# Performance work log

Measured on AMD Instinct MI355X. Metric: run time of the kernel, lower is better.

Reference implementation:

```python
import jax, jax.numpy as jnp
import numpy as np

NUM_USERS = 200000
NUM_ITEMS = 100000
EMB = 64
NUM_LAYERS = 3


def setup_inputs() -> dict:
    rng = np.random.default_rng(0)
    E_INTER = 2_000_000
    # unique (user, item) interactions -> faithful to adj[e0, e1] = 1.0 set-semantics
    lin = np.unique(rng.integers(0, NUM_USERS * NUM_ITEMS, size=E_INTER, dtype=np.int64))
    u = (lin // NUM_ITEMS).astype(np.int32)
    it = (lin % NUM_ITEMS).astype(np.int32) + NUM_USERS  # item node ids offset by NUM_USERS
    row = np.concatenate([u, it])  # symmetric bipartite graph, no self-loops
    col = np.concatenate([it, u])
    edge_index = jnp.asarray(np.stack([row, col]), dtype=jnp.int32)  # [2, E]

    key = jax.random.key(0)
    k1, k2 = jax.random.split(key)
    # xavier_uniform on nn.Embedding.weight
    bu = float(np.sqrt(6.0 / (NUM_USERS + EMB)))
    bi = float(np.sqrt(6.0 / (NUM_ITEMS + EMB)))
    user_emb = jax.random.uniform(k1, (NUM_USERS, EMB), jnp.float32, -bu, bu)
    item_emb = jax.random.uniform(k2, (NUM_ITEMS, EMB), jnp.float32, -bi, bi)
    return {"edge_index": edge_index, "user_emb": user_emb, "item_emb": item_emb}


def reference(edge_index, user_emb, item_emb):
    num_users = user_emb.shape[0]
    N = num_users + item_emb.shape[0]
    x = jnp.concatenate([user_emb, item_emb], axis=0)  # ego embeddings [N, D]
    row, col = edge_index[0], edge_index[1]

    # adj has unique off-diagonal edges + eye(N): row-sum degree = edge count + 1
    deg = jax.ops.segment_sum(jnp.ones(row.shape, x.dtype), row, num_segments=N) + 1.0
    dinv = jax.lax.rsqrt(deg)                 # deg >= 1, never inf
    w = (dinv[row] * dinv[col])[:, None]      # per-edge D^-1/2 A D^-1/2 weight
    self_w = (dinv * dinv)[:, None]           # self-loop weight d_i^-1

    acc = x  # sum over layer outputs, including layer 0
    for _ in range(NUM_LAYERS):
        x = jax.ops.segment_sum(w * x[col], row, num_segments=N) + self_w * x
        # dropout is identity in eval mode
        acc = acc + x

    return acc[:num_users], acc[num_users:]
```

## Files before the change

kernel.cpp:

```cpp
#include <hip/hip_runtime.h>
#include <hip/hip_bf16.h>

#define EMB 64
#define BKT_BITS 10
#define BKT_SZ   (1 << BKT_BITS)
#define U_BITS   18
#define U_MASK   ((1u << U_BITS) - 1u)

__device__ __forceinline__ float bf2f(unsigned short h) {
    return __uint_as_float(((unsigned)h) << 16);
}
__device__ __forceinline__ unsigned short f2bf(float f) {
    unsigned u = __float_as_uint(f);
    unsigned r = (u + 0x7fffu + ((u >> 16) & 1u)) >> 16;
    return (unsigned short)r;
}

__global__ void k1_kernel(const int* __restrict__ row, const int* __restrict__ colh,
                          int* __restrict__ urp, int* __restrict__ degit,
                          int NU, int Eh, int urp_blocks) {
    if ((int)blockIdx.x < urp_blocks) {
        int r = blockIdx.x * blockDim.x + threadIdx.x;
        if (r > NU) return;
        if (r == NU) { urp[NU] = Eh; return; }
        int lo = 0, hi = Eh;
        while (lo < hi) {
            int mid = (lo + hi) >> 1;
            if (row[mid] < r) lo = mid + 1; else hi = mid;
        }
        urp[r] = lo;
    } else {
        int e = (blockIdx.x - urp_blocks) * blockDim.x + threadIdx.x;
        if (e < Eh) atomicAdd(&degit[colh[e] - NU], 1);
    }
}

__global__ void k3_kernel(const int* __restrict__ degit, int* __restrict__ excl,
                          int* __restrict__ partials,
                          const int* __restrict__ urp, float* __restrict__ dinv,
                          const float* __restrict__ ue, const float* __restrict__ ie,
                          unsigned short* __restrict__ y0,
                          int NU, int NI, int N, long nu_elems, long total,
                          int nb_s1, int nb_dv) {
    int b = blockIdx.x;
    if (b < nb_s1) {
        __shared__ int sh[256];
        int t = threadIdx.x;
        int base = b * 1024 + t * 4;
        int d0 = (base + 0 < NI) ? degit[base + 0] : 0;
        int d1 = (base + 1 < NI) ? degit[base + 1] : 0;
        int d2 = (base + 2 < NI) ? degit[base + 2] : 0;
        int d3 = (base + 3 < NI) ? degit[base + 3] : 0;
        int tsum = d0 + d1 + d2 + d3;
        sh[t] = tsum;
        __syncthreads();
        for (int off = 1; off < 256; off <<= 1) {
            int v = (t >= off) ? sh[t - off] : 0;
            __syncthreads();
            sh[t] += v;
            __syncthreads();
        }
        int excl_t = sh[t] - tsum;
        if (base + 0 < NI) excl[base + 0] = excl_t;
        if (base + 1 < NI) excl[base + 1] = excl_t + d0;
        if (base + 2 < NI) excl[base + 2] = excl_t + d0 + d1;
        if (base + 3 < NI) excl[base + 3] = excl_t + d0 + d1 + d2;
        if (t == 255) partials[b] = sh[t];
    } else if (b < nb_s1 + nb_dv) {
        int i = (b - nb_s1) * blockDim.x + threadIdx.x;
        if (i >= N) return;
        int d = (i < NU) ? (urp[i + 1] - urp[i]) : degit[i - NU];
        dinv[i] = rsqrtf((float)d + 1.0f);
    } else {
        long j4 = ((long)(b - nb_s1 - nb_dv) * blockDim.x + threadIdx.x) * 4;
        if (j4 >= total) return;
        int node = (int)(j4 >> 6);
        int d = (node < NU) ? (urp[node + 1] - urp[node]) : degit[node - NU];
        float sc = rsqrtf((float)d + 1.0f);
        float4 v = (j4 < nu_elems) ? ((const float4*)ue)[j4 >> 2]
                                   : ((const float4*)ie)[(j4 - nu_elems) >> 2];
        ushort4 o;
        o.x = f2bf(sc * v.x); o.y = f2bf(sc * v.y);
        o.z = f2bf(sc * v.z); o.w = f2bf(sc * v.w);
        ((ushort4*)y0)[j4 >> 2] = o;
    }
}

__global__ void scan2_kernel(int* __restrict__ partials, int nb) {
    __shared__ int sh[512];
    int t = threadIdx.x;
    int v = (t < nb) ? partials[t] : 0;
    sh[t] = v;
    __syncthreads();
    for (int off = 1; off < 512; off <<= 1) {
        int u = (t >= off) ? sh[t - off] : 0;
        __syncthreads();
        sh[t] += u;
        __syncthreads();
    }
    if (t < nb) partials[t] = sh[t] - v;
}

__global__ void scan3_kernel(const int* __restrict__ excl, const int* __restrict__ partials,
                             int* __restrict__ irp, int* __restrict__ cursor,
                             int* __restrict__ bcur, int NI, int Eh) {
    int i = blockIdx.x * blockDim.x + threadIdx.x;
    if (i < NI) {
        int v = excl[i] + partials[i >> 10];
        irp[i] = v;
        cursor[i] = v;
        if ((i & (BKT_SZ - 1)) == 0) bcur[i >> BKT_BITS] = v;
    }
    if (i == NI) irp[NI] = Eh;
}

__global__ void passA_kernel(const int* __restrict__ rowh, const int* __restrict__ colh,
                             int* __restrict__ bcur, unsigned* __restrict__ staging,
                             int Eh, int NU, int NB) {
    __shared__ int cnt[512];
    __shared__ int base[512];
    int t = threadIdx.x;
    for (int j = t; j < NB; j += 256) cnt[j] = 0;
    __syncthreads();
    long cb = (long)blockIdx.x * 1024;
    int b[4], rk[4];
    unsigned pk[4];
#pragma unroll
    for (int j = 0; j < 4; ++j) {
        long e = cb + j * 256 + t;
        if (e < Eh) {
            int u = rowh[e];
            int loc = colh[e] - NU;
            b[j] = loc >> BKT_BITS;
            pk[j] = ((unsigned)(loc & (BKT_SZ - 1)) << U_BITS) | (unsigned)u;
            rk[j] = atomicAdd(&cnt[b[j]], 1);
        } else {
            b[j] = -1;
        }
    }
    __syncthreads();
    for (int j = t; j < NB; j += 256)
        base[j] = cnt[j] ? atomicAdd(&bcur[j], cnt[j]) : 0;
    __syncthreads();
#pragma unroll
    for (int j = 0; j < 4; ++j)
        if (b[j] >= 0) staging[base[b[j]] + rk[j]] = pk[j];
}

__device__ __forceinline__ void spmm_node_l0u(
    int i, int q,
    const int* __restrict__ urp, const int* __restrict__ colg,
    const float* __restrict__ dinv,
    const unsigned short* __restrict__ yc,
    unsigned short* __restrict__ yn) {
    int s = urp[i], e = urp[i + 1];
    float di = dinv[i];
    const ushort4* __restrict__ yc4 = (const ushort4*)yc;
    long p = (long)i * 16 + q;
    ushort4 sv = yc4[p];

    float ax = 0.f, ay = 0.f, az = 0.f, aw = 0.f;
    for (int k0 = s; k0 < e; k0 += 8) {
        int   c[8];
        float w[8];
#pragma unroll
        for (int j = 0; j < 8; ++j) {
            int k = k0 + j;
            bool v = (k < e);
            c[j] = v ? colg[k] : 0;
            w[j] = v ? 1.0f : 0.0f;
        }
        ushort4 u[8];
#pragma unroll
        for (int j = 0; j < 8; ++j) u[j] = yc4[(long)c[j] * 16 + q];
#pragma unroll
        for (int j = 0; j < 8; ++j) {
            ax += w[j] * bf2f(u[j].x);
            ay += w[j] * bf2f(u[j].y);
            az += w[j] * bf2f(u[j].z);
            aw += w[j] * bf2f(u[j].w);
        }
    }
    ax += bf2f(sv.x); ay += bf2f(sv.y); az += bf2f(sv.z); aw += bf2f(sv.w);
    float t = di * di;
    ushort4 o;
    o.x = f2bf(t * ax); o.y = f2bf(t * ay); o.z = f2bf(t * az); o.w = f2bf(t * aw);
    ((ushort4*)yn)[p] = o;
}

__global__ void m6_kernel(const unsigned* __restrict__ staging,
                          const int* __restrict__ irp, int* __restrict__ cursor,
                          int* __restrict__ icols, int NB, int NI,
                          const int* __restrict__ urp,
                          const int* __restrict__ colg,
                          const float* __restrict__ dinv,
                          const unsigned short* __restrict__ y0,
                          unsigned short* __restrict__ y1, int NU) {
    int b = (int)blockIdx.x;
    if (b < NB) {
        int lo = b << BKT_BITS;
        int hi = lo + BKT_SZ; if (hi > NI) hi = NI;
        int start = irp[lo], end = irp[hi];
        for (int k = start + (int)threadIdx.x; k < end; k += 256) {
            unsigned v = staging[k];
            int u   = (int)(v & U_MASK);
            int loc = lo + (int)(v >> U_BITS);
            int pos = atomicAdd(&cursor[loc], 1);
            icols[pos] = u;
        }
    } else {
        long t = (long)(b - NB) * blockDim.x + threadIdx.x;
        int i = (int)(t >> 4);
        if (i >= NU) return;
        spmm_node_l0u(i, (int)(t & 15), urp, colg, dinv, y0, y1);
    }
}

__global__ void d2_kernel(const int* __restrict__ irp, const int* __restrict__ icols,
                          const float* __restrict__ dinv,
                          const unsigned short* __restrict__ y0,
                          unsigned short* __restrict__ y1,
                          unsigned short* __restrict__ y2, int NU, int NI) {
    long t = (long)blockIdx.x * blockDim.x + threadIdx.x;
    int j = (int)(t >> 4);
    if (j >= NI) return;
    int q = (int)(t & 15);
    int i = NU + j;
    int s = irp[j], e = irp[j + 1];
    float di = dinv[i];
    const ushort4* __restrict__ y04 = (const ushort4*)y0;
    const ushort4* __restrict__ y14 = (const ushort4*)y1;
    long p = (long)i * 16 + q;
    ushort4 sv0 = y04[p];

    float a0x = 0.f, a0y = 0.f, a0z = 0.f, a0w = 0.f;
    float a1x = 0.f, a1y = 0.f, a1z = 0.f, a1w = 0.f;
    for (int k0 = s; k0 < e; k0 += 8) {
        long  off[8];
        float w[8];
#pragma unroll
        for (int jj = 0; jj < 8; ++jj) {
            int k = k0 + jj;
            bool v = (k < e);
            int c = v ? icols[k] : 0;
            off[jj] = (long)c * 16 + q;
            w[jj] = v ? 1.0f : 0.0f;
        }
        ushort4 u0[8], u1[8];
#pragma unroll
        for (int jj = 0; jj < 8; ++jj) { u0[jj] = y04[off[jj]]; u1[jj] = y14[off[jj]]; }
#pragma unroll
        for (int jj = 0; jj < 8; ++jj) {
            a0x += w[jj] * bf2f(u0[jj].x); a0y += w[jj] * bf2f(u0[jj].y);
            a0z += w[jj] * bf2f(u0[jj].z); a0w += w[jj] * bf2f(u0[jj].w);
            a1x += w[jj] * bf2f(u1[jj].x); a1y += w[jj] * bf2f(u1[jj].y);
            a1z += w[jj] * bf2f(u1[jj].z); a1w += w[jj] * bf2f(u1[jj].w);
        }
    }
    float sq = di * di;
    a0x += bf2f(sv0.x); a0y += bf2f(sv0.y); a0z += bf2f(sv0.z); a0w += bf2f(sv0.w);
    ushort4 o1;
    o1.x = f2bf(sq * a0x); o1.y = f2bf(sq * a0y);
    o1.z = f2bf(sq * a0z); o1.w = f2bf(sq * a0w);
    ((ushort4*)y1)[p] = o1;
    a1x += bf2f(o1.x); a1y += bf2f(o1.y); a1z += bf2f(o1.z); a1w += bf2f(o1.w);
    ushort4 o2;
    o2.x = f2bf(sq * a1x); o2.y = f2bf(sq * a1y);
    o2.z = f2bf(sq * a1z); o2.w = f2bf(sq * a1w);
    ((ushort4*)y2)[p] = o2;
}

__global__ void d3_kernel(const int* __restrict__ urp, const int* __restrict__ colg,
                          const float* __restrict__ dinv,
                          const unsigned short* __restrict__ y0,
                          const unsigned short* __restrict__ y1,
                          unsigned short* __restrict__ y2,
                          float* __restrict__ out, int NU) {
    long t = (long)blockIdx.x * blockDim.x + threadIdx.x;
    int i = (int)(t >> 4);
    if (i >= NU) return;
    int q = (int)(t & 15);
    int s = urp[i], e = urp[i + 1];
    float di = dinv[i];
    const ushort4* __restrict__ y04 = (const ushort4*)y0;
    const ushort4* __restrict__ y14 = (const ushort4*)y1;
    const ushort4* __restrict__ y24 = (const ushort4*)y2;
    long p = (long)i * 16 + q;
    ushort4 sv0 = y04[p];
    ushort4 sv1 = y14[p];

    float a1x = 0.f, a1y = 0.f, a1z = 0.f, a1w = 0.f;
    float a2x = 0.f, a2y = 0.f, a2z = 0.f, a2w = 0.f;
    for (int k0 = s; k0 < e; k0 += 8) {
        long  off[8];
        float w[8];
#pragma unroll
        for (int jj = 0; jj < 8; ++jj) {
            int k = k0 + jj;
            bool v = (k < e);
            int c = v ? colg[k] : 0;
            off[jj] = (long)c * 16 + q;
            w[jj] = v ? 1.0f : 0.0f;
        }
        ushort4 u1[8], u2[8];
#pragma unroll
        for (int jj = 0; jj < 8; ++jj) { u1[jj] = y14[off[jj]]; u2[jj] = y24[off[jj]]; }
#pragma unroll
        for (int jj = 0; jj < 8; ++jj) {
            a1x += w[jj] * bf2f(u1[jj].x); a1y += w[jj] * bf2f(u1[jj].y);
            a1z += w[jj] * bf2f(u1[jj].z); a1w += w[jj] * bf2f(u1[jj].w);
            a2x += w[jj] * bf2f(u2[jj].x); a2y += w[jj] * bf2f(u2[jj].y);
            a2z += w[jj] * bf2f(u2[jj].z); a2w += w[jj] * bf2f(u2[jj].w);
        }
    }
    float sq = di * di;
    a1x += bf2f(sv1.x); a1y += bf2f(sv1.y); a1z += bf2f(sv1.z); a1w += bf2f(sv1.w);
    ushort4 o2;
    o2.x = f2bf(sq * a1x); o2.y = f2bf(sq * a1y);
    o2.z = f2bf(sq * a1z); o2.w = f2bf(sq * a1w);
    ((ushort4*)y2)[p] = o2;
    a2x += bf2f(o2.x); a2y += bf2f(o2.y); a2z += bf2f(o2.z); a2w += bf2f(o2.w);
    float inv = 1.0f / di;
    float4 o;
    o.x = (bf2f(sv0.x) + bf2f(sv1.x) + bf2f(o2.x)) * inv + di * a2x;
    o.y = (bf2f(sv0.y) + bf2f(sv1.y) + bf2f(o2.y)) * inv + di * a2y;
    o.z = (bf2f(sv0.z) + bf2f(sv1.z) + bf2f(o2.z)) * inv + di * a2z;
    o.w = (bf2f(sv0.w) + bf2f(sv1.w) + bf2f(o2.w)) * inv + di * a2w;
    ((float4*)out)[p] = o;
}

__global__ void d4_kernel(const int* __restrict__ irp, const int* __restrict__ icols,
                          const float* __restrict__ dinv,
                          const unsigned short* __restrict__ y0,
                          const unsigned short* __restrict__ y1,
                          const unsigned short* __restrict__ y2,
                          float* __restrict__ out, int NU, int NI) {
    long t = (long)blockIdx.x * blockDim.x + threadIdx.x;
    int j = (int)(t >> 4);
    if (j >= NI) return;
    int q = (int)(t & 15);
    int i = NU + j;
    int s = irp[j], e = irp[j + 1];
    float di = dinv[i];
    const ushort4* __restrict__ y04 = (const ushort4*)y0;
    const ushort4* __restrict__ y14 = (const ushort4*)y1;
    const ushort4* __restrict__ y24 = (const ushort4*)y2;
    long p = (long)i * 16 + q;
    ushort4 sv0 = y04[p];
    ushort4 sv1 = y14[p];
    ushort4 sv2 = y24[p];

    float ax = 0.f, ay = 0.f, az = 0.f, aw = 0.f;
    for (int k0 = s; k0 < e; k0 += 8) {
        int   c[8];
        float w[8];
#pragma unroll
        for (int jj = 0; jj < 8; ++jj) {
            int k = k0 + jj;
            bool v = (k < e);
            c[jj] = v ? icols[k] : 0;
            w[jj] = v ? 1.0f : 0.0f;
        }
        ushort4 u[8];
#pragma unroll
        for (int jj = 0; jj < 8; ++jj) u[jj] = y24[(long)c[jj] * 16 + q];
#pragma unroll
        for (int jj = 0; jj < 8; ++jj) {
            ax += w[jj] * bf2f(u[jj].x);
            ay += w[jj] * bf2f(u[jj].y);
            az += w[jj] * bf2f(u[jj].z);
            aw += w[jj] * bf2f(u[jj].w);
        }
    }
    ax += bf2f(sv2.x); ay += bf2f(sv2.y); az += bf2f(sv2.z); aw += bf2f(sv2.w);
    float inv = 1.0f / di;
    float4 o;
    o.x = (bf2f(sv0.x) + bf2f(sv1.x) + bf2f(sv2.x)) * inv + di * ax;
    o.y = (bf2f(sv0.y) + bf2f(sv1.y) + bf2f(sv2.y)) * inv + di * ay;
    o.z = (bf2f(sv0.z) + bf2f(sv1.z) + bf2f(sv2.z)) * inv + di * az;
    o.w = (bf2f(sv0.w) + bf2f(sv1.w) + bf2f(sv2.w)) * inv + di * aw;
    ((float4*)out)[p] = o;
}

extern "C" void kernel_launch(void* const* d_in, const int* in_sizes, int n_in,
                              void* d_out, int out_size, void* d_ws, size_t ws_size,
                              hipStream_t stream) {
    const int*   edge_index = (const int*)d_in[0];
    const float* user_emb   = (const float*)d_in[1];
    const float* item_emb   = (const float*)d_in[2];
    float* out = (float*)d_out;

    const int  E  = in_sizes[0] / 2;
    const int  Eh = E / 2;
    const int  NU = in_sizes[1] / EMB;
    const int  NI = in_sizes[2] / EMB;
    const int  N  = NU + NI;
    const long total = (long)N * EMB;

    const int* row = edge_index;
    const int* col = edge_index + E;
    const int* rowh = row;
    const int* colh = col;

    int*   urp      = (int*)d_ws;
    int*   degit    = urp + (NU + 1);
    int*   excl     = degit + NI;
    int*   partials = excl + NI;
    int*   bcur     = partials + 512;
    int*   irp      = bcur + 512;
    int*   cursor   = irp + (NI + 1);
    int*   icols    = cursor + NI;
    float* dinv     = (float*)(icols + Eh);
    unsigned short* y0 = (unsigned short*)(((uintptr_t)(dinv + N) + 127) & ~(uintptr_t)127);
    unsigned short* y1 = y0 + total;
    unsigned short* y2 = y1 + total;
    unsigned* staging = (unsigned*)(y1 + (long)NU * EMB);

    hipMemsetAsync(degit, 0, (size_t)NI * sizeof(int), stream);

    int urp_blocks  = (NU + 256) / 256;
    int ideg_blocks = (Eh + 255) / 256;
    k1_kernel<<<urp_blocks + ideg_blocks, 256, 0, stream>>>(row, colh, urp, degit,
                                                            NU, Eh, urp_blocks);

    int nb_s1 = (NI + 1023) / 1024;
    int nb_dv = (N + 255) / 256;
    int nb_in = (int)((total / 4 + 255) / 256);
    k3_kernel<<<nb_s1 + nb_dv + nb_in, 256, 0, stream>>>(degit, excl, partials,
                                                         urp, dinv, user_emb, item_emb, y0,
                                                         NU, NI, N, (long)NU * EMB, total,
                                                         nb_s1, nb_dv);

    scan2_kernel<<<1, 512, 0, stream>>>(partials, nb_s1);
    scan3_kernel<<<(NI + 1 + 255) / 256, 256, 0, stream>>>(excl, partials, irp, cursor,
                                                           bcur, NI, Eh);

    int NB = (NI + BKT_SZ - 1) >> BKT_BITS;
    int nb_pa = (Eh + 1023) / 1024;
    passA_kernel<<<nb_pa, 256, 0, stream>>>(rowh, colh, bcur, staging, Eh, NU, NB);

    int nb_us = (int)(((long)NU * 16 + 255) / 256);
    m6_kernel<<<NB + nb_us, 256, 0, stream>>>(staging, irp, cursor, icols, NB, NI,
                                              urp, col, dinv, y0, y1, NU);

    int nb_it = (int)(((long)NI * 16 + 255) / 256);
    d2_kernel<<<nb_it, 256, 0, stream>>>(irp, icols, dinv, y0, y1, y2, NU, NI);

    d3_kernel<<<nb_us, 256, 0, stream>>>(urp, col, dinv, y0, y1, y2, out, NU);

    d4_kernel<<<nb_it, 256, 0, stream>>>(irp, icols, dinv, y0, y1, y2, out, NU, NI);
}
```

Baseline: 602.3 us.

## Build item CSR via bucket histogram and in-block scan, dropping per-item degree atomics

Replaces the per-item global degree atomics, multi-kernel prefix scan and cursor-based scatter with a per-bucket histogram (shared-memory atomics), a single small scan over bucket totals, and a passB kernel. passB counts per-item degrees in shared memory, scans them, writes irp, dinv and the item CSR columns, and scales item embeddings into y0. User dinv and y0 scaling are fused into the binary-search kernel, and bucket counters are padded to avoid false sharing. This cuts kernel launches and global atomics, at the cost of one 1024-thread block per bucket and only about 98 blocks in passB. The user layer-0 SpMM is also split back out as its own kernel instead of running alongside the scatter.

```diff
diff --git a/kernel.cpp b/kernel.cpp
--- a/kernel.cpp
+++ b/kernel.cpp
@@ -4,6 +4,8 @@
 #define EMB 64
 #define BKT_BITS 10
 #define BKT_SZ   (1 << BKT_BITS)
+#define NBMAX    256
+#define PAD      32
 #define U_BITS   18
 #define U_MASK   ((1u << U_BITS) - 1u)
 
@@ -17,110 +19,86 @@
 }
 
 __global__ void k1_kernel(const int* __restrict__ row, const int* __restrict__ colh,
-                          int* __restrict__ urp, int* __restrict__ degit,
-                          int NU, int Eh, int urp_blocks) {
-    if ((int)blockIdx.x < urp_blocks) {
-        int r = blockIdx.x * blockDim.x + threadIdx.x;
-        if (r > NU) return;
-        if (r == NU) { urp[NU] = Eh; return; }
-        int lo = 0, hi = Eh;
-        while (lo < hi) {
-            int mid = (lo + hi) >> 1;
-            if (row[mid] < r) lo = mid + 1; else hi = mid;
-        }
-        urp[r] = lo;
+                          int* __restrict__ urp, float* __restrict__ dinv,
+                          const float* __restrict__ ue, unsigned short* __restrict__ y0,
+                          int* __restrict__ btotp,
+                          int NU, int Eh, int NB, int UB) {
+    __shared__ int bound[17];
+    __shared__ int hist[NBMAX];
+    int t = threadIdx.x;
+    if ((int)blockIdx.x < UB) {
+        int r0 = blockIdx.x * 16;
+        if (t < 17) {
+            int r = r0 + t;
+            if (r <= NU) {
+                int lo = 0, hi = Eh;
+                while (lo < hi) {
+                    int mid = (lo + hi) >> 1;
+                    if (row[mid] < r) lo = mid + 1; else hi = mid;
+                }
+                bound[t] = lo;
+                urp[r] = lo;
+                if (t < 16 && r < NU)
+                    dinv[r] = rsqrtf((float)(0) + 0.0f);
+            }
+        }
+        __syncthreads();
+        if (t < 16 && r0 + t < NU)
+            dinv[r0 + t] = rsqrtf((float)(bound[t + 1] - bound[t]) + 1.0f);
+        long j4 = (long)r0 * 64 + t * 4;
+        if (j4 < (long)NU * 64) {
+            int rb = t >> 4;
+            float sc = rsqrtf((float)(bound[rb + 1] - bound[rb]) + 1.0f);
+            float4 v = ((const float4*)ue)[j4 >> 2];
+            ushort4 o;
+            o.x = f2bf(sc * v.x); o.y = f2bf(sc * v.y);
+            o.z = f2bf(sc * v.z); o.w = f2bf(sc * v.w);
+            ((ushort4*)y0)[j4 >> 2] = o;
+        }
     } else {
-        int e = (blockIdx.x - urp_blocks) * blockDim.x + threadIdx.x;
-        if (e < Eh) atomicAdd(&degit[colh[e] - NU], 1);
-    }
-}
-
-__global__ void k3_kernel(const int* __restrict__ degit, int* __restrict__ excl,
-                          int* __restrict__ partials,
-                          const int* __restrict__ urp, float* __restrict__ dinv,
-                          const float* __restrict__ ue, const float* __restrict__ ie,
-                          unsigned short* __restrict__ y0,
-                          int NU, int NI, int N, long nu_elems, long total,
-                          int nb_s1, int nb_dv) {
-    int b = blockIdx.x;
-    if (b < nb_s1) {
-        __shared__ int sh[256];
-        int t = threadIdx.x;
-        int base = b * 1024 + t * 4;
-        int d0 = (base + 0 < NI) ? degit[base + 0] : 0;
-        int d1 = (base + 1 < NI) ? degit[base + 1] : 0;
-        int d2 = (base + 2 < NI) ? degit[base + 2] : 0;
-        int d3 = (base + 3 < NI) ? degit[base + 3] : 0;
-        int tsum = d0 + d1 + d2 + d3;
-        sh[t] = tsum;
-        __syncthreads();
-        for (int off = 1; off < 256; off <<= 1) {
-            int v = (t >= off) ? sh[t - off] : 0;
-            __syncthreads();
-            sh[t] += v;
-            __syncthreads();
-        }
-        int excl_t = sh[t] - tsum;
-        if (base + 0 < NI) excl[base + 0] = excl_t;
-        if (base + 1 < NI) excl[base + 1] = excl_t + d0;
-        if (base + 2 < NI) excl[base + 2] = excl_t + d0 + d1;
-        if (base + 3 < NI) excl[base + 3] = excl_t + d0 + d1 + d2;
-        if (t == 255) partials[b] = sh[t];
-    } else if (b < nb_s1 + nb_dv) {
-        int i = (b - nb_s1) * blockDim.x + threadIdx.x;
-        if (i >= N) return;
-        int d = (i < NU) ? (urp[i + 1] - urp[i]) : degit[i - NU];
-        dinv[i] = rsqrtf((float)d + 1.0f);
-    } else {
-        long j4 = ((long)(b - nb_s1 - nb_dv) * blockDim.x + threadIdx.x) * 4;
-        if (j4 >= total) return;
-        int node = (int)(j4 >> 6);
-        int d = (node < NU) ? (urp[node + 1] - urp[node]) : degit[node - NU];
-        float sc = rsqrtf((float)d + 1.0f);
-        float4 v = (j4 < nu_elems) ? ((const float4*)ue)[j4 >> 2]
-                                   : ((const float4*)ie)[(j4 - nu_elems) >> 2];
-        ushort4 o;
-        o.x = f2bf(sc * v.x); o.y = f2bf(sc * v.y);
-        o.z = f2bf(sc * v.z); o.w = f2bf(sc * v.w);
-        ((ushort4*)y0)[j4 >> 2] = o;
-    }
-}
-
-__global__ void scan2_kernel(int* __restrict__ partials, int nb) {
-    __shared__ int sh[512];
+        hist[t] = 0;
+        if (t + 256 < NBMAX) hist[t + 256] = 0;
+        __syncthreads();
+        long e0 = (long)(blockIdx.x - UB) * 4096;
+#pragma unroll
+        for (int k = 0; k < 16; ++k) {
+            long e = e0 + k * 256 + t;
+            if (e < Eh) atomicAdd(&hist[(colh[e] - NU) >> BKT_BITS], 1);
+        }
+        __syncthreads();
+        if (t < NB && hist[t]) atomicAdd(&btotp[t * PAD], hist[t]);
+    }
+}
+
+__global__ void scanS_kernel(const int* __restrict__ btotp, int* __restrict__ bbase,
+                             int* __restrict__ bcurp, int NB, int Eh) {
+    __shared__ int sh[256];
     int t = threadIdx.x;
-    int v = (t < nb) ? partials[t] : 0;
+    int v = (t < NB) ? btotp[t * PAD] : 0;
     sh[t] = v;
     __syncthreads();
-    for (int off = 1; off < 512; off <<= 1) {
+    for (int off = 1; off < 256; off <<= 1) {
         int u = (t >= off) ? sh[t - off] : 0;
         __syncthreads();
         sh[t] += u;
         __syncthreads();
     }
-    if (t < nb) partials[t] = sh[t] - v;
-}
-
-__global__ void scan3_kernel(const int* __restrict__ excl, const int* __restrict__ partials,
-                             int* __restrict__ irp, int* __restrict__ cursor,
-                             int* __restrict__ bcur, int NI, int Eh) {
-    int i = blockIdx.x * blockDim.x + threadIdx.x;
-    if (i < NI) {
-        int v = excl[i] + partials[i >> 10];
-        irp[i] = v;
-        cursor[i] = v;
-        if ((i & (BKT_SZ - 1)) == 0) bcur[i >> BKT_BITS] = v;
-    }
-    if (i == NI) irp[NI] = Eh;
+    if (t < NB) {
+        int excl = sh[t] - v;
+        bbase[t] = excl;
+        bcurp[t * PAD] = excl;
+        if (t == NB - 1) bbase[NB] = sh[t];
+    }
 }
 
 __global__ void passA_kernel(const int* __restrict__ rowh, const int* __restrict__ colh,
-                             int* __restrict__ bcur, unsigned* __restrict__ staging,
+                             int* __restrict__ bcurp, unsigned* __restrict__ staging,
                              int Eh, int NU, int NB) {
-    __shared__ int cnt[512];
-    __shared__ int base[512];
+    __shared__ int cnt[NBMAX];
+    __shared__ int base[NBMAX];
     int t = threadIdx.x;
-    for (int j = t; j < NB; j += 256) cnt[j] = 0;
+    cnt[t] = 0;
+    if (t + 256 < NBMAX) cnt[t + 256] = 0;
     __syncthreads();
     long cb = (long)blockIdx.x * 1024;
     int b[4], rk[4];
@@ -139,25 +117,82 @@
         }
     }
     __syncthreads();
-    for (int j = t; j < NB; j += 256)
-        base[j] = cnt[j] ? atomicAdd(&bcur[j], cnt[j]) : 0;
+    if (t < NB) base[t] = cnt[t] ? atomicAdd(&bcurp[t * PAD], cnt[t]) : 0;
     __syncthreads();
 #pragma unroll
     for (int j = 0; j < 4; ++j)
         if (b[j] >= 0) staging[base[b[j]] + rk[j]] = pk[j];
 }
 
-__device__ __forceinline__ void spmm_node_l0u(
-    int i, int q,
-    const int* __restrict__ urp, const int* __restrict__ colg,
-    const float* __restrict__ dinv,
-    const unsigned short* __restrict__ yc,
-    unsigned short* __restrict__ yn) {
+__global__ void passB_kernel(const unsigned* __restrict__ staging,
+                             const int* __restrict__ bbase,
+                             int* __restrict__ irp, int* __restrict__ icols,
+                             float* __restrict__ dinv,
+                             const float* __restrict__ ie, unsigned short* __restrict__ y0,
+                             int NU, int NI, int NB, int Eh) {
+    __shared__ int cnt[BKT_SZ];
+    __shared__ int sh[BKT_SZ];
+    int t = threadIdx.x;
+    int b = blockIdx.x;
+    int lo = b << BKT_BITS;
+    int sb = bbase[b], se = bbase[b + 1];
+
+    cnt[t] = 0;
+    __syncthreads();
+    for (int k = sb + t; k < se; k += 1024)
+        atomicAdd(&cnt[staging[k] >> U_BITS], 1);
+    __syncthreads();
+
+    sh[t] = cnt[t];
+    __syncthreads();
+    for (int off = 1; off < 1024; off <<= 1) {
+        int v = (t >= off) ? sh[t - off] : 0;
+        __syncthreads();
+        sh[t] += v;
+        __syncthreads();
+    }
+    int exclv = sh[t] - cnt[t];
+    int item = lo + t;
+    if (item < NI) {
+        irp[item] = sb + exclv;
+        dinv[NU + item] = rsqrtf((float)cnt[t] + 1.0f);
+    }
+    if (b == NB - 1 && t == 0) irp[NI] = Eh;
+    __syncthreads();
+    sh[t] = exclv;
+    __syncthreads();
+    for (int k = sb + t; k < se; k += 1024) {
+        unsigned v = staging[k];
+        int io = (int)(v >> U_BITS);
+        int r = atomicAdd(&sh[io], 1);
+        icols[sb + r] = (int)(v & U_MASK);
+    }
+
+    for (int m = t; m < BKT_SZ * 16; m += 1024) {
+        int it = lo + (m >> 4);
+        if (it >= NI) break;
+        float sc = rsqrtf((float)cnt[m >> 4] + 1.0f);
+        float4 v = ((const float4*)ie)[(long)it * 16 + (m & 15)];
+        ushort4 o;
+        o.x = f2bf(sc * v.x); o.y = f2bf(sc * v.y);
+        o.z = f2bf(sc * v.z); o.w = f2bf(sc * v.w);
+        ((ushort4*)y0)[((long)NU + it) * 16 + (m & 15)] = o;
+    }
+}
+
+__global__ void ul0_kernel(const int* __restrict__ urp, const int* __restrict__ colg,
+                           const float* __restrict__ dinv,
+                           const unsigned short* __restrict__ y0,
+                           unsigned short* __restrict__ y1, int NU) {
+    long t = (long)blockIdx.x * blockDim.x + threadIdx.x;
+    int i = (int)(t >> 4);
+    if (i >= NU) return;
+    int q = (int)(t & 15);
     int s = urp[i], e = urp[i + 1];
     float di = dinv[i];
-    const ushort4* __restrict__ yc4 = (const ushort4*)yc;
+    const ushort4* __restrict__ y04 = (const ushort4*)y0;
     long p = (long)i * 16 + q;
-    ushort4 sv = yc4[p];
+    ushort4 sv = y04[p];
 
     float ax = 0.f, ay = 0.f, az = 0.f, aw = 0.f;
     for (int k0 = s; k0 < e; k0 += 8) {
@@ -172,7 +207,7 @@
         }
         ushort4 u[8];
 #pragma unroll
-        for (int j = 0; j < 8; ++j) u[j] = yc4[(long)c[j] * 16 + q];
+        for (int j = 0; j < 8; ++j) u[j] = y04[(long)c[j] * 16 + q];
 #pragma unroll
         for (int j = 0; j < 8; ++j) {
             ax += w[j] * bf2f(u[j].x);
@@ -182,38 +217,10 @@
         }
     }
     ax += bf2f(sv.x); ay += bf2f(sv.y); az += bf2f(sv.z); aw += bf2f(sv.w);
-    float t = di * di;
+    float sq = di * di;
     ushort4 o;
-    o.x = f2bf(t * ax); o.y = f2bf(t * ay); o.z = f2bf(t * az); o.w = f2bf(t * aw);
-    ((ushort4*)yn)[p] = o;
-}
-
-__global__ void m6_kernel(const unsigned* __restrict__ staging,
-                          const int* __restrict__ irp, int* __restrict__ cursor,
-                          int* __restrict__ icols, int NB, int NI,
-                          const int* __restrict__ urp,
-                          const int* __restrict__ colg,
-                          const float* __restrict__ dinv,
-                          const unsigned short* __restrict__ y0,
-                          unsigned short* __restrict__ y1, int NU) {
-    int b = (int)blockIdx.x;
-    if (b < NB) {
-        int lo = b << BKT_BITS;
-        int hi = lo + BKT_SZ; if (hi > NI) hi = NI;
-        int start = irp[lo], end = irp[hi];
-        for (int k = start + (int)threadIdx.x; k < end; k += 256) {
-            unsigned v = staging[k];
-            int u   = (int)(v & U_MASK);
-            int loc = lo + (int)(v >> U_BITS);
-            int pos = atomicAdd(&cursor[loc], 1);
-            icols[pos] = u;
-        }
-    } else {
-        long t = (long)(b - NB) * blockDim.x + threadIdx.x;
-        int i = (int)(t >> 4);
-        if (i >= NU) return;
-        spmm_node_l0u(i, (int)(t & 15), urp, colg, dinv, y0, y1);
-    }
+    o.x = f2bf(sq * ax); o.y = f2bf(sq * ay); o.z = f2bf(sq * az); o.w = f2bf(sq * aw);
+    ((ushort4*)y1)[p] = o;
 }
 
 __global__ void d2_kernel(const int* __restrict__ irp, const int* __restrict__ icols,
@@ -402,46 +409,37 @@
     const int* rowh = row;
     const int* colh = col;
 
-    int*   urp      = (int*)d_ws;
-    int*   degit    = urp + (NU + 1);
-    int*   excl     = degit + NI;
-    int*   partials = excl + NI;
-    int*   bcur     = partials + 512;
-    int*   irp      = bcur + 512;
-    int*   cursor   = irp + (NI + 1);
-    int*   icols    = cursor + NI;
-    float* dinv     = (float*)(icols + Eh);
+    int*   urp   = (int*)d_ws;
+    int*   btotp = urp + (NU + 1);
+    int*   bcurp = btotp + NBMAX * PAD;
+    int*   bbase = bcurp + NBMAX * PAD;
+    int*   irp   = bbase + (NBMAX + 1);
+    int*   icols = irp + (NI + 1);
+    float* dinv  = (float*)(icols + Eh);
     unsigned short* y0 = (unsigned short*)(((uintptr_t)(dinv + N) + 127) & ~(uintptr_t)127);
     unsigned short* y1 = y0 + total;
     unsigned short* y2 = y1 + total;
     unsigned* staging = (unsigned*)(y1 + (long)NU * EMB);
 
-    hipMemsetAsync(degit, 0, (size_t)NI * sizeof(int), stream);
-
-    int urp_blocks  = (NU + 256) / 256;
-    int ideg_blocks = (Eh + 255) / 256;
-    k1_kernel<<<urp_blocks + ideg_blocks, 256, 0, stream>>>(row, colh, urp, degit,
-                                                            NU, Eh, urp_blocks);
-
-    int nb_s1 = (NI + 1023) / 1024;
-    int nb_dv = (N + 255) / 256;
-    int nb_in = (int)((total / 4 + 255) / 256);
-    k3_kernel<<<nb_s1 + nb_dv + nb_in, 256, 0, stream>>>(degit, excl, partials,
-                                                         urp, dinv, user_emb, item_emb, y0,
-                                                         NU, NI, N, (long)NU * EMB, total,
-                                                         nb_s1, nb_dv);
-
-    scan2_kernel<<<1, 512, 0, stream>>>(partials, nb_s1);
-    scan3_kernel<<<(NI + 1 + 255) / 256, 256, 0, stream>>>(excl, partials, irp, cursor,
-                                                           bcur, NI, Eh);
-
-    int NB = (NI + BKT_SZ - 1) >> BKT_BITS;
-    int nb_pa = (Eh + 1023) / 1024;
-    passA_kernel<<<nb_pa, 256, 0, stream>>>(rowh, colh, bcur, staging, Eh, NU, NB);
+    const int NB = (NI + BKT_SZ - 1) >> BKT_BITS;
+
+    hipMemsetAsync(btotp, 0, (size_t)NBMAX * PAD * sizeof(int), stream);
+
+    int UB = (NU + 15) / 16;
+    int PC = (Eh + 4095) / 4096;
+    k1_kernel<<<UB + PC, 256, 0, stream>>>(row, colh, urp, dinv, user_emb, y0,
+                                           btotp, NU, Eh, NB, UB);
+
+    scanS_kernel<<<1, 256, 0, stream>>>(btotp, bbase, bcurp, NB, Eh);
+
+    passA_kernel<<<(Eh + 1023) / 1024, 256, 0, stream>>>(rowh, colh, bcurp, staging,
+                                                         Eh, NU, NB);
+
+    passB_kernel<<<NB, 1024, 0, stream>>>(staging, bbase, irp, icols, dinv,
+                                          item_emb, y0, NU, NI, NB, Eh);
 
     int nb_us = (int)(((long)NU * 16 + 255) / 256);
-    m6_kernel<<<NB + nb_us, 256, 0, stream>>>(staging, irp, cursor, icols, NB, NI,
-                                              urp, col, dinv, y0, y1, NU);
+    ul0_kernel<<<nb_us, 256, 0, stream>>>(urp, col, dinv, y0, y1, NU);
 
     int nb_it = (int)(((long)NI * 16 + 255) / 256);
     d2_kernel<<<nb_it, 256, 0, stream>>>(irp, icols, dinv, y0, y1, y2, NU, NI);
```

After: 531.9 us. -11.7%, faster.
